# Optimization experiments

Hardware: AMD Instinct MI355X
Metric: run time of the kernel (lower is better)

The kernel has to match this reference:

```python
import jax, jax.numpy as jnp
import numpy as np
from jax import lax

H = W = 96
C = 3
N_PIX = H * W
N_PER_CLASS = 50   # min(size_sample_fg=100 -> shuffled to min_samples, size_sample_bg=50)
K = 5
THRESHOLD = 0.3
POS_WEIGHT = 100.0
CLEAN_THRESH = 0.6


def _sample_idx(key, valid_mask_flat, n):
    # Uniform random sample of n indices from valid positions (fixed-shape
    # replacement for tf.random.shuffle(tf.where(mask))[:n]).
    u = jax.random.uniform(key, (N_PIX,))
    score = jnp.where(valid_mask_flat, u, -1.0)
    _, idx = lax.top_k(score, n)
    return idx


def _pixel_features(img01):
    # img01: [H, W, C] in [0, 1]. Matches: reshape(img)/255 concat weighted positions.
    img_flat = img01.reshape(-1, C) / 255.0
    ii, jj = jnp.meshgrid(jnp.arange(H), jnp.arange(W), indexing='ij')
    pos = jnp.stack([ii, jj], axis=-1).reshape(-1, 2).astype(jnp.float32)
    pos = pos / jnp.array([H, W], jnp.float32) * POS_WEIGHT
    return jnp.concatenate([img_flat, pos], axis=1)  # [N_PIX, C+2]


def _process_image(img, key):
    # preprocess: (already 96x96x3) normalize & clip
    img_p = jnp.clip(img / 255.0, 0.0, 1.0)

    # extract_image_tf: clean image, pick fg/bg scribble pixels
    img_norm = img_p / jnp.max(img_p, axis=(0, 1), keepdims=True)
    cleaned = img_norm * (img_norm < CLEAN_THRESH).astype(jnp.float32)
    fg = jnp.any(cleaned > 0, axis=-1).reshape(-1)  # [N_PIX] bool
    bg = ~fg
    k_fg, k_bg = jax.random.split(key)
    fg_idx = _sample_idx(k_fg, fg, N_PER_CLASS)
    bg_idx = _sample_idx(k_bg, bg, N_PER_CLASS)

    # extract_features_tf
    feats_all = _pixel_features(img_p)                       # [N_PIX, 5]
    train_feats = jnp.concatenate([feats_all[fg_idx], feats_all[bg_idx]], axis=0)  # [100, 5]
    train_labels = jnp.concatenate([jnp.ones(N_PER_CLASS), jnp.zeros(N_PER_CLASS)])

    # segment_image_KNN_tf: standardize, brute-force cdist, top-k, label vote
    mean = jnp.mean(train_feats, axis=0)
    std = jnp.std(train_feats, axis=0)
    train_s = (train_feats - mean) / std                     # [100, 5]
    test_s = (feats_all - mean) / std                        # [N_PIX, 5]
    dist = jnp.sqrt(jnp.sum(jnp.square(test_s[:, None, :] - train_s[None, :, :]), axis=2))  # [N_PIX, 100]
    _, knn_idx = lax.top_k(-dist, K)                         # smallest-k distances
    probas = jnp.mean(train_labels[knn_idx], axis=1)         # [N_PIX]
    seg = (probas >= THRESHOLD).astype(jnp.int32).reshape(H, W)

    # mask original (preprocessed) image
    return jnp.where(seg[..., None] == 1, img_p, jnp.zeros_like(img_p))


def setup_inputs() -> dict:
    key = jax.random.key(0)
    images = jax.random.uniform(key, (32, H, W, C), dtype=jnp.float32)
    return {"images": images}


def reference(images):
    B = images.shape[0]
    keys = jax.random.split(jax.random.key(42), B)
    return jax.vmap(_process_image)(images, keys)
```

## Files before the change

### kernel.cpp

```cpp
#include <hip/hip_runtime.h>
#include <stdint.h>

#define NPIX 9216
#define NIMG 32
#define STRIP 1152

__device__ __forceinline__ uint32_t rotl32(uint32_t x, int d){ return (x<<d)|(x>>(32-d)); }

__device__ __forceinline__ void threefry(uint32_t k0, uint32_t k1, uint32_t x0, uint32_t x1,
                                         uint32_t &o0, uint32_t &o1){
  uint32_t ks2 = k0 ^ k1 ^ 0x1BD11BDAu;
  x0 += k0; x1 += k1;
  x0+=x1; x1=rotl32(x1,13); x1^=x0;
  x0+=x1; x1=rotl32(x1,15); x1^=x0;
  x0+=x1; x1=rotl32(x1,26); x1^=x0;
  x0+=x1; x1=rotl32(x1,6);  x1^=x0;
  x0+=k1; x1+=ks2+1u;
  x0+=x1; x1=rotl32(x1,17); x1^=x0;
  x0+=x1; x1=rotl32(x1,29); x1^=x0;
  x0+=x1; x1=rotl32(x1,16); x1^=x0;
  x0+=x1; x1=rotl32(x1,24); x1^=x0;
  x0+=ks2; x1+=k0+2u;
  x0+=x1; x1=rotl32(x1,13); x1^=x0;
  x0+=x1; x1=rotl32(x1,15); x1^=x0;
  x0+=x1; x1=rotl32(x1,26); x1^=x0;
  x0+=x1; x1=rotl32(x1,6);  x1^=x0;
  x0+=k0; x1+=k1+3u;
  x0+=x1; x1=rotl32(x1,17); x1^=x0;
  x0+=x1; x1=rotl32(x1,29); x1^=x0;
  x0+=x1; x1=rotl32(x1,16); x1^=x0;
  x0+=x1; x1=rotl32(x1,24); x1^=x0;
  x0+=k1; x1+=ks2+4u;
  x0+=x1; x1=rotl32(x1,13); x1^=x0;
  x0+=x1; x1=rotl32(x1,15); x1^=x0;
  x0+=x1; x1=rotl32(x1,26); x1^=x0;
  x0+=x1; x1=rotl32(x1,6);  x1^=x0;
  x0+=ks2; x1+=k0+5u;
  o0=x0; o1=x1;
}

__device__ __forceinline__ float clip01_div255(float x){
  return fminf(fmaxf(x/255.0f, 0.0f), 1.0f);
}

__global__ __launch_bounds__(256) void kmax(const float* __restrict__ in,
                                            float* __restrict__ maxpart){
  int img  = blockIdx.x / 6;
  int part = blockIdx.x % 6;
  int tid  = threadIdx.x;
  const float* base = in + (size_t)img*NPIX*3 + (size_t)part*1536*3;
  float m0=0.f, m1=0.f, m2=0.f;
#pragma unroll
  for(int k=0;k<18;k++){
    int g = k*256 + tid;
    float v = clip01_div255(base[g]);
    int c = g % 3;
    m0 = (c==0) ? fmaxf(m0,v) : m0;
    m1 = (c==1) ? fmaxf(m1,v) : m1;
    m2 = (c==2) ? fmaxf(m2,v) : m2;
  }
  for(int off=32; off>0; off>>=1){
    m0 = fmaxf(m0, __shfl_down(m0,off));
    m1 = fmaxf(m1, __shfl_down(m1,off));
    m2 = fmaxf(m2, __shfl_down(m2,off));
  }
  __shared__ float r[3][4];
  int lane = tid & 63, wv = tid >> 6;
  if(lane==0){ r[0][wv]=m0; r[1][wv]=m1; r[2][wv]=m2; }
  __syncthreads();
  if(tid==0){
    maxpart[blockIdx.x*3+0]=fmaxf(fmaxf(r[0][0],r[0][1]),fmaxf(r[0][2],r[0][3]));
    maxpart[blockIdx.x*3+1]=fmaxf(fmaxf(r[1][0],r[1][1]),fmaxf(r[1][2],r[1][3]));
    maxpart[blockIdx.x*3+2]=fmaxf(fmaxf(r[2][0],r[2][1]),fmaxf(r[2][2],r[2][3]));
  }
}

__global__ __launch_bounds__(256) void kscore(const float* __restrict__ in,
                                              const float* __restrict__ maxpart,
                                              unsigned long long* __restrict__ key50g){
#pragma clang fp contract(off)
  int b   = blockIdx.x;
  int img = b >> 4, cls = (b >> 3) & 1, sub = b & 7;
  int tid = threadIdx.x;

  __shared__ __attribute__((aligned(16))) float pixL[3456];
  __shared__ uint32_t vvL[STRIP];
  __shared__ uint64_t cand[STRIP];
  __shared__ int hist[129];
  __shared__ int ncand, bbin;

  if(tid<129) hist[tid]=0;
  if(tid==0)  ncand=0;

  const float* p = in + (size_t)img*NPIX*3;

  const float4* sp4 = (const float4*)(p + (size_t)sub*STRIP*3);
  float4* pixL4 = (float4*)pixL;
  for(int k=0;k<4;k++){ int i4=k*256+tid; if(i4<864) pixL4[i4]=sp4[i4]; }

  float c0=0.f,c1=0.f,c2=0.f;
#pragma unroll
  for(int s=0;s<6;s++){
    c0=fmaxf(c0, maxpart[(img*6+s)*3+0]);
    c1=fmaxf(c1, maxpart[(img*6+s)*3+1]);
    c2=fmaxf(c2, maxpart[(img*6+s)*3+2]);
  }

  uint32_t ik0, ik1; threefry(0u, 42u, 0u, (uint32_t)img, ik0, ik1);
  uint32_t s0, s1;   threefry(ik0, ik1, 0u, (uint32_t)cls, s0, s1);
  __syncthreads();

  for(int r=0;r<5;r++){
    int pi = tid + r*256;
    if(pi<STRIP){
      float a  = clip01_div255(pixL[pi*3+0])/c0;
      float bb = clip01_div255(pixL[pi*3+1])/c1;
      float c  = clip01_div255(pixL[pi*3+2])/c2;
      bool fg = (a>0.f && a<0.6f) || (bb>0.f && bb<0.6f) || (c>0.f && c<0.6f);
      bool valid = (cls==0) ? fg : !fg;
      uint32_t gi = (uint32_t)(sub*STRIP + pi);
      uint32_t r1,r2; threefry(s0, s1, 0u, gi, r1, r2);
      uint32_t vv = valid ? ((r1 ^ r2) >> 9) + 1u : 0u;
      vvL[pi] = vv;
      atomicAdd(&hist[vv>>16], 1);
    }
  }
  __syncthreads();
  if(tid==0){
    int acc=0, bx=128;
    for(; bx>=0; bx--){ acc += hist[bx]; if(acc>=50) break; }
    bbin = bx;
  }
  __syncthreads();
  int bb = bbin;
  for(int r=0;r<5;r++){
    int pi = tid + r*256;
    if(pi<STRIP){
      uint32_t vv = vvL[pi];
      if((int)(vv>>16) >= bb){
        int pos = atomicAdd(&ncand,1);
        cand[pos] = ((uint64_t)vv << 14) | (uint64_t)(16383 - (sub*STRIP + pi));
      }
    }
  }
  __syncthreads();
  int m = ncand;
  for(int c=tid;c<m;c+=256){
    uint64_t k = cand[c];
    int r = 0, j = 0;
    while(j < m){
      int je = j+64 < m ? j+64 : m;
      for(; j<je; j++) r += (cand[j] > k);
      if(r >= 50) break;
    }
    if(r < 50) key50g[(size_t)b*50 + r] = k;
  }
}

__global__ __launch_bounds__(256) void kmerge(const float* __restrict__ in,
                                              const unsigned long long* __restrict__ key50g,
                                              float* __restrict__ ts2g,
                                              float* __restrict__ meanstd){
#pragma clang fp contract(off)
  int img = blockIdx.x;
  int tid = threadIdx.x;
  __shared__ uint64_t kk[800];
  __shared__ int      tIdx[100];
  __shared__ float    feat[100][5];
  __shared__ float    mv[5], sv[5];

  const uint64_t* kg = (const uint64_t*)key50g + (size_t)img*800;
  for(int c=tid;c<800;c+=256) kk[c] = kg[c];
  __syncthreads();

  for(int c=tid;c<800;c+=256){
    uint64_t k = kk[c];
    int cl = (c >= 400);
    int base = cl*400;
    int r = 0;
#pragma unroll
    for(int s=0;s<8;s++){
      const uint64_t* L = &kk[base + s*50];
      int lo=0, hi=50;
      while(lo<hi){ int mid=(lo+hi)>>1; if(L[mid] > k) lo=mid+1; else hi=mid; }
      r += lo;
    }
    if(r < 50) tIdx[cl*50+r] = 16383 - (int)(k & 16383u);
  }
  __syncthreads();

  if(tid<100){
    int pp = tIdx[tid];
    int i=pp/96, j=pp-i*96;
    const float* px = in + ((size_t)img*NPIX + pp)*3;
    for(int c=0;c<3;c++){
      float ip=clip01_div255(px[c]);
      feat[tid][c]=ip/255.0f;
    }
    feat[tid][3]=((float)i/96.0f)*100.0f;
    feat[tid][4]=((float)j/96.0f)*100.0f;
  }
  __syncthreads();
  if(tid<5){
    float s=0.f;
    for(int r=0;r<100;r++) s=s+feat[r][tid];
    float mu=s/100.0f; mv[tid]=mu;
    float v=0.f;
    for(int r=0;r<100;r++){ float d=feat[r][tid]-mu; float q=d*d; v=v+q; }
    sv[tid]=sqrtf(v/100.0f);
  }
  __syncthreads();
  if(tid<100){
    float r0=(feat[tid][0]-mv[0])/sv[0];
    float r1=(feat[tid][1]-mv[1])/sv[1];
    float r2=(feat[tid][2]-mv[2])/sv[2];
    float r3=(feat[tid][3]-mv[3])/sv[3];
    float r4=(feat[tid][4]-mv[4])/sv[4];
    float* dst = ts2g + img*600 + (tid>>1)*12 + (tid&1)*5;
    dst[0]=r0; dst[1]=r1; dst[2]=r2; dst[3]=r3; dst[4]=r4;
  }
  if(tid<5)       meanstd[img*10+tid]=mv[tid];
  else if(tid<10) meanstd[img*10+tid]=sv[tid-5];
}

__global__ __launch_bounds__(256) void kknn(const float* __restrict__ in,
                                            const float* __restrict__ ts2g,
                                            const float* __restrict__ meanstd,
                                            float* __restrict__ out){
#pragma clang fp contract(off)
  int b     = blockIdx.x;
  int img   = b / 36;
  int chunk = b % 36;
  int tid   = threadIdx.x;

  __shared__ float    mv[5], sv[5];
  __shared__ __attribute__((aligned(16))) float ts2[600];
  __shared__ __attribute__((aligned(16))) float pix[768];

  if(tid<150) ((float4*)ts2)[tid] = ((const float4*)(ts2g + img*600))[tid];
  if(tid>=192 && tid<197) mv[tid-192]=meanstd[img*10+(tid-192)];
  if(tid>=224 && tid<229) sv[tid-224]=meanstd[img*10+5+(tid-224)];
  {
    const float4* cb4 = (const float4*)(in + ((size_t)img*NPIX + (size_t)chunk*256)*3);
    if(tid<192) ((float4*)pix)[tid] = cb4[tid];
  }
  __syncthreads();

  int p = chunk*256+tid;
  int i=p/96, j=p-i*96;
  float ip0=clip01_div255(pix[tid*3+0]);
  float ip1=clip01_div255(pix[tid*3+1]);
  float ip2=clip01_div255(pix[tid*3+2]);
  float t0,t1,t2,t3,t4;
  {
    float f0=ip0/255.0f, f1=ip1/255.0f, f2=ip2/255.0f;
    float f3=((float)i/96.0f)*100.0f, f4=((float)j/96.0f)*100.0f;
    t0=(f0-mv[0])/sv[0]; t1=(f1-mv[1])/sv[1]; t2=(f2-mv[2])/sv[2];
    t3=(f3-mv[3])/sv[3]; t4=(f4-mv[4])/sv[4];
  }

  float a0=1e30f,a1=1e30f;
#pragma unroll 5
  for(int pr=0;pr<25;pr++){
    const float* tp = &ts2[pr*12];
    float4 qa = *(const float4*)(tp);
    float4 qb = *(const float4*)(tp+4);
    float2 qc = *(const float2*)(tp+8);
    {
      float s;
      { float d=t0-qa.x; s=d*d; }
      { float d=t1-qa.y; float w=d*d; s=s+w; }
      { float d=t2-qa.z; float w=d*d; s=s+w; }
      { float d=t3-qa.w; float w=d*d; s=s+w; }
      { float d=t4-qb.x; float w=d*d; s=s+w; }
      bool l0=s<a0,l1=s<a1;
      a1 = l1 ? (l0?a0:s) : a1;
      a0 = l0 ? s : a0;
    }
    {
      float s;
      { float d=t0-qb.y; s=d*d; }
      { float d=t1-qb.z; float w=d*d; s=s+w; }
      { float d=t2-qb.w; float w=d*d; s=s+w; }
      { float d=t3-qc.x; float w=d*d; s=s+w; }
      { float d=t4-qc.y; float w=d*d; s=s+w; }
      bool l0=s<a0,l1=s<a1;
      a1 = l1 ? (l0?a0:s) : a1;
      a0 = l0 ? s : a0;
    }
  }
  float b0=1e30f,b1=1e30f,b2=1e30f,b3=1e30f;
#pragma unroll 5
  for(int pr=25;pr<50;pr++){
    const float* tp = &ts2[pr*12];
    float4 qa = *(const float4*)(tp);
    float4 qb = *(const float4*)(tp+4);
    float2 qc = *(const float2*)(tp+8);
    {
      float s;
      { float d=t0-qa.x; s=d*d; }
      { float d=t1-qa.y; float w=d*d; s=s+w; }
      { float d=t2-qa.z; float w=d*d; s=s+w; }
      { float d=t3-qa.w; float w=d*d; s=s+w; }
      { float d=t4-qb.x; float w=d*d; s=s+w; }
      bool l0=s<b0,l1=s<b1,l2=s<b2,l3=s<b3;
      b3 = l3 ? (l2?b2:s) : b3;
      b2 = l2 ? (l1?b1:s) : b2;
      b1 = l1 ? (l0?b0:s) : b1;
      b0 = l0 ? s : b0;
    }
    {
      float s;
      { float d=t0-qb.y; s=d*d; }
      { float d=t1-qb.z; float w=d*d; s=s+w; }
      { float d=t2-qb.w; float w=d*d; s=s+w; }
      { float d=t3-qc.x; float w=d*d; s=s+w; }
      { float d=t4-qc.y; float w=d*d; s=s+w; }
      bool l0=s<b0,l1=s<b1,l2=s<b2,l3=s<b3;
      b3 = l3 ? (l2?b2:s) : b3;
      b2 = l2 ? (l1?b1:s) : b2;
      b1 = l1 ? (l0?b0:s) : b1;
      b0 = l0 ? s : b0;
    }
  }
  bool seg = sqrtf(a1) <= sqrtf(b3);
  __syncthreads();
  pix[tid*3+0]=seg?ip0:0.f;
  pix[tid*3+1]=seg?ip1:0.f;
  pix[tid*3+2]=seg?ip2:0.f;
  __syncthreads();
  float4* ob4 = (float4*)(out + ((size_t)img*NPIX + (size_t)chunk*256)*3);
  if(tid<192) ob4[tid] = ((float4*)pix)[tid];
}

extern "C" void kernel_launch(void* const* d_in, const int* in_sizes, int n_in,
                              void* d_out, int out_size, void* d_ws, size_t ws_size,
                              hipStream_t stream) {
  const float* in = (const float*)d_in[0];
  float* out = (float*)d_out;
  float* maxpart = (float*)d_ws;
  unsigned long long* key50g = (unsigned long long*)((char*)d_ws + 2304);
  float* ts2g    = (float*)((char*)d_ws + 207104);
  float* meanstd = (float*)((char*)d_ws + 283904);

  kmax  <<<192,  256, 0, stream>>>(in, maxpart);
  kscore<<<512,  256, 0, stream>>>(in, maxpart, key50g);
  kmerge<<<32,   256, 0, stream>>>(in, key50g, ts2g, meanstd);
  kknn  <<<1152, 256, 0, stream>>>(in, ts2g, meanstd, out);
}
```

Baseline: 113.6 us.

## Fuse merge into score kernel via last-block ticket; split KNN top-k chains

Removes the separate merge kernel launch. The last of the 16 score blocks per image, found through an atomic ticket counter, now performs the 800-key merge and the standardisation. The score kernel also issues its global pixel loads and threefry RNG before the shared-memory store so they overlap. The KNN kernel splits each running top-k insertion into two independent chains that are combined at the end, which shortens the dependency chain. The ticket relies on a workspace sentinel reset trick and adds threadfence costs and serial tail work in one block per image.

```diff
diff --git a/kernel.cpp b/kernel.cpp
--- a/kernel.cpp
+++ b/kernel.cpp
@@ -77,7 +77,10 @@
 
 __global__ __launch_bounds__(256) void kscore(const float* __restrict__ in,
                                               const float* __restrict__ maxpart,
-                                              unsigned long long* __restrict__ key50g){
+                                              unsigned long long* __restrict__ key50g,
+                                              int* __restrict__ ticket,
+                                              float* __restrict__ ts2g,
+                                              float* __restrict__ meanstd){
 #pragma clang fp contract(off)
   int b   = blockIdx.x;
   int img = b >> 4, cls = (b >> 3) & 1, sub = b & 7;
@@ -87,7 +90,10 @@
   __shared__ uint32_t vvL[STRIP];
   __shared__ uint64_t cand[STRIP];
   __shared__ int hist[129];
-  __shared__ int ncand, bbin;
+  __shared__ int ncand, bbin, myold;
+  __shared__ int   tIdx[100];
+  __shared__ float feat[100][5];
+  __shared__ float mv[5], sv[5];
 
   if(tid<129) hist[tid]=0;
   if(tid==0)  ncand=0;
@@ -95,8 +101,10 @@
   const float* p = in + (size_t)img*NPIX*3;
 
   const float4* sp4 = (const float4*)(p + (size_t)sub*STRIP*3);
-  float4* pixL4 = (float4*)pixL;
-  for(int k=0;k<4;k++){ int i4=k*256+tid; if(i4<864) pixL4[i4]=sp4[i4]; }
+  float4 st0 = sp4[tid];
+  float4 st1 = sp4[256+tid];
+  float4 st2 = sp4[512+tid];
+  float4 st3 = (tid<96) ? sp4[768+tid] : make_float4(0.f,0.f,0.f,0.f);
 
   float c0=0.f,c1=0.f,c2=0.f;
 #pragma unroll
@@ -108,8 +116,24 @@
 
   uint32_t ik0, ik1; threefry(0u, 42u, 0u, (uint32_t)img, ik0, ik1);
   uint32_t s0, s1;   threefry(ik0, ik1, 0u, (uint32_t)cls, s0, s1);
-  __syncthreads();
-
+  uint32_t rng[5];
+#pragma unroll
+  for(int r=0;r<5;r++){
+    int pi = tid + r*256;
+    if(pi < STRIP){
+      uint32_t r1,r2; threefry(s0, s1, 0u, (uint32_t)(sub*STRIP+pi), r1, r2);
+      rng[r] = r1 ^ r2;
+    }
+  }
+
+  float4* pixL4 = (float4*)pixL;
+  pixL4[tid]     = st0;
+  pixL4[256+tid] = st1;
+  pixL4[512+tid] = st2;
+  if(tid<96) pixL4[768+tid] = st3;
+  __syncthreads();
+
+#pragma unroll
   for(int r=0;r<5;r++){
     int pi = tid + r*256;
     if(pi<STRIP){
@@ -118,9 +142,7 @@
       float c  = clip01_div255(pixL[pi*3+2])/c2;
       bool fg = (a>0.f && a<0.6f) || (bb>0.f && bb<0.6f) || (c>0.f && c<0.6f);
       bool valid = (cls==0) ? fg : !fg;
-      uint32_t gi = (uint32_t)(sub*STRIP + pi);
-      uint32_t r1,r2; threefry(s0, s1, 0u, gi, r1, r2);
-      uint32_t vv = valid ? ((r1 ^ r2) >> 9) + 1u : 0u;
+      uint32_t vv = valid ? (rng[r] >> 9) + 1u : 0u;
       vvL[pi] = vv;
       atomicAdd(&hist[vv>>16], 1);
     }
@@ -155,21 +177,20 @@
     }
     if(r < 50) key50g[(size_t)b*50 + r] = k;
   }
-}
-
-__global__ __launch_bounds__(256) void kmerge(const float* __restrict__ in,
-                                              const unsigned long long* __restrict__ key50g,
-                                              float* __restrict__ ts2g,
-                                              float* __restrict__ meanstd){
-#pragma clang fp contract(off)
-  int img = blockIdx.x;
-  int tid = threadIdx.x;
-  __shared__ uint64_t kk[800];
-  __shared__ int      tIdx[100];
-  __shared__ float    feat[100][5];
-  __shared__ float    mv[5], sv[5];
-
+
+  __threadfence();
+  __syncthreads();
+  if(tid==0){
+    atomicCAS(&ticket[img], (int)0xAAAAAAAA, 0);
+    myold = atomicAdd(&ticket[img], 1);
+  }
+  __syncthreads();
+  if(myold != 15) return;
+
+  __threadfence();
+  uint64_t* kk = cand;
   const uint64_t* kg = (const uint64_t*)key50g + (size_t)img*800;
+  __syncthreads();
   for(int c=tid;c<800;c+=256) kk[c] = kg[c];
   __syncthreads();
 
@@ -259,7 +280,7 @@
     t3=(f3-mv[3])/sv[3]; t4=(f4-mv[4])/sv[4];
   }
 
-  float a0=1e30f,a1=1e30f;
+  float aE0=1e30f,aE1=1e30f, aO0=1e30f,aO1=1e30f;
 #pragma unroll 5
   for(int pr=0;pr<25;pr++){
     const float* tp = &ts2[pr*12];
@@ -273,9 +294,9 @@
       { float d=t2-qa.z; float w=d*d; s=s+w; }
       { float d=t3-qa.w; float w=d*d; s=s+w; }
       { float d=t4-qb.x; float w=d*d; s=s+w; }
-      bool l0=s<a0,l1=s<a1;
-      a1 = l1 ? (l0?a0:s) : a1;
-      a0 = l0 ? s : a0;
+      bool l0=s<aE0,l1=s<aE1;
+      aE1 = l1 ? (l0?aE0:s) : aE1;
+      aE0 = l0 ? s : aE0;
     }
     {
       float s;
@@ -284,12 +305,15 @@
       { float d=t2-qb.w; float w=d*d; s=s+w; }
       { float d=t3-qc.x; float w=d*d; s=s+w; }
       { float d=t4-qc.y; float w=d*d; s=s+w; }
-      bool l0=s<a0,l1=s<a1;
-      a1 = l1 ? (l0?a0:s) : a1;
-      a0 = l0 ? s : a0;
-    }
-  }
-  float b0=1e30f,b1=1e30f,b2=1e30f,b3=1e30f;
+      bool l0=s<aO0,l1=s<aO1;
+      aO1 = l1 ? (l0?aO0:s) : aO1;
+      aO0 = l0 ? s : aO0;
+    }
+  }
+  float a1 = fmaxf(fminf(aE0,aO1), fminf(aE1,aO0));
+
+  float bP0=1e30f,bP1=1e30f,bP2=1e30f,bP3=1e30f;
+  float bQ0=1e30f,bQ1=1e30f,bQ2=1e30f,bQ3=1e30f;
 #pragma unroll 5
   for(int pr=25;pr<50;pr++){
     const float* tp = &ts2[pr*12];
@@ -303,11 +327,11 @@
       { float d=t2-qa.z; float w=d*d; s=s+w; }
       { float d=t3-qa.w; float w=d*d; s=s+w; }
       { float d=t4-qb.x; float w=d*d; s=s+w; }
-      bool l0=s<b0,l1=s<b1,l2=s<b2,l3=s<b3;
-      b3 = l3 ? (l2?b2:s) : b3;
-      b2 = l2 ? (l1?b1:s) : b2;
-      b1 = l1 ? (l0?b0:s) : b1;
-      b0 = l0 ? s : b0;
+      bool l0=s<bP0,l1=s<bP1,l2=s<bP2,l3=s<bP3;
+      bP3 = l3 ? (l2?bP2:s) : bP3;
+      bP2 = l2 ? (l1?bP1:s) : bP2;
+      bP1 = l1 ? (l0?bP0:s) : bP1;
+      bP0 = l0 ? s : bP0;
     }
     {
       float s;
@@ -316,13 +340,16 @@
       { float d=t2-qb.w; float w=d*d; s=s+w; }
       { float d=t3-qc.x; float w=d*d; s=s+w; }
       { float d=t4-qc.y; float w=d*d; s=s+w; }
-      bool l0=s<b0,l1=s<b1,l2=s<b2,l3=s<b3;
-      b3 = l3 ? (l2?b2:s) : b3;
-      b2 = l2 ? (l1?b1:s) : b2;
-      b1 = l1 ? (l0?b0:s) : b1;
-      b0 = l0 ? s : b0;
-    }
-  }
+      bool l0=s<bQ0,l1=s<bQ1,l2=s<bQ2,l3=s<bQ3;
+      bQ3 = l3 ? (l2?bQ2:s) : bQ3;
+      bQ2 = l2 ? (l1?bQ1:s) : bQ2;
+      bQ1 = l1 ? (l0?bQ0:s) : bQ1;
+      bQ0 = l0 ? s : bQ0;
+    }
+  }
+  float l0=fminf(bP0,bQ3), l1=fminf(bP1,bQ2), l2=fminf(bP2,bQ1), l3=fminf(bP3,bQ0);
+  float b3 = fmaxf(fmaxf(l0,l1), fmaxf(l2,l3));
+
   bool seg = sqrtf(a1) <= sqrtf(b3);
   __syncthreads();
   pix[tid*3+0]=seg?ip0:0.f;
@@ -340,11 +367,11 @@
   float* out = (float*)d_out;
   float* maxpart = (float*)d_ws;
   unsigned long long* key50g = (unsigned long long*)((char*)d_ws + 2304);
-  float* ts2g    = (float*)((char*)d_ws + 207104);
-  float* meanstd = (float*)((char*)d_ws + 283904);
+  int*   ticket  = (int*)((char*)d_ws + 207104);
+  float* ts2g    = (float*)((char*)d_ws + 207232);
+  float* meanstd = (float*)((char*)d_ws + 284032);
 
   kmax  <<<192,  256, 0, stream>>>(in, maxpart);
-  kscore<<<512,  256, 0, stream>>>(in, maxpart, key50g);
-  kmerge<<<32,   256, 0, stream>>>(in, key50g, ts2g, meanstd);
+  kscore<<<512,  256, 0, stream>>>(in, maxpart, key50g, ticket, ts2g, meanstd);
   kknn  <<<1152, 256, 0, stream>>>(in, ts2g, meanstd, out);
 }
```

New measurement: 133.8 us. 17.8% more time.
